# Optimization experiments

Measured on AMD Instinct MI355X. Metric: run time of the kernel, lower is better.

The kernel has to match this reference:

```python
import jax, jax.numpy as jnp
import numpy as np

B, L, DIM, HEADS = 4, 1024, 512, 8
HD = DIM // HEADS
HID = max(64, DIM // 2)
WIN = 32
SPARSITY = 0.3
TEMP = 1.0
PAT_TAU = 0.5


def setup_inputs() -> dict:
    key = jax.random.key(0)
    ks = jax.random.split(key, 8)
    gn = lambda k, shape, sc: jax.random.normal(k, shape, jnp.float32) * sc
    return {
        "x": jax.random.normal(ks[0], (B, L, DIM), jnp.float32),
        "mask": jnp.ones((B, L), jnp.int32),
        "Wqkv": gn(ks[1], (3 * DIM, DIM), 0.02),
        "Wproj": gn(ks[2], (DIM, DIM), 0.02),
        "bproj": jnp.zeros((DIM,), jnp.float32),
        "Wsel1": gn(ks[3], (HID, DIM), 0.05),
        "bsel1": jnp.zeros((HID,), jnp.float32),
        "Wsel2": gn(ks[4], (3, HID), 0.05),
        "bsel2": jnp.zeros((3,), jnp.float32),
        "log_pattern_tau": jnp.asarray(np.log(PAT_TAU), jnp.float32),
        "sparse_w": gn(ks[5], (HEADS,), 0.2),
        "sparse_b": jnp.zeros((HEADS,), jnp.float32),
    }


def reference(x, mask, Wqkv, Wproj, bproj, Wsel1, bsel1, Wsel2, bsel2,
              log_pattern_tau, sparse_w, sparse_b):
    Bq, Lq, D = x.shape
    scale = HD ** -0.5
    qkv = (x @ Wqkv.T).reshape(Bq, Lq, 3, HEADS, HD)
    q = jnp.transpose(qkv[:, :, 0], (0, 2, 1, 3))  # (B,H,L,hd)
    k = jnp.transpose(qkv[:, :, 1], (0, 2, 1, 3))
    v = jnp.transpose(qkv[:, :, 2], (0, 2, 1, 3))
    scores = jnp.einsum('bhid,bhjd->bhij', q, k) * scale  # (B,H,L,L)

    # pattern selector on mean-pooled features (eval: no gumbel, no dropout)
    pooled = x.mean(axis=1)
    logits = jax.nn.relu(pooled @ Wsel1.T + bsel1) @ Wsel2.T + bsel2  # (B,3)
    tau = jnp.clip(jnp.exp(log_pattern_tau), 1e-4, 10.0)
    pw = jax.nn.softmax(logits / tau, axis=-1)  # (B,3)

    half = WIN // 2
    ii = jnp.arange(Lq)[:, None]
    jj = jnp.arange(Lq)[None, :]
    local = ((jj >= ii - half) & (jj <= ii + half)).astype(jnp.float32)

    # learned sparse top-k mask per head via kth-value threshold
    kk = max(1, int(Lq * (1.0 - SPARSITY)))
    s = scores * sparse_w[None, :, None, None] + sparse_b[None, :, None, None]
    kth = jax.lax.top_k(s, kk)[0][..., -1:]
    smask = (s >= kth).astype(jnp.float32)  # (B,H,L,L)

    combined = (pw[:, 0, None, None, None] * local[None, None]
                + pw[:, 1, None, None, None]
                + pw[:, 2, None, None, None] * smask)
    neg = jnp.float32(-1e9)
    scores = jnp.where(combined > 0.05, scores, neg)
    scores = jnp.where(mask[:, None, None, :] == 0, neg, scores)

    # fallback: if a row is fully masked, unmask position 0
    all_masked = jnp.all(scores <= neg + 1e-6, axis=-1)  # (B,H,L)
    scores = scores.at[..., 0].set(jnp.where(all_masked, 0.0, scores[..., 0]))

    attn = jax.nn.softmax(scores / TEMP, axis=-1)
    out = jnp.einsum('bhij,bhjd->bhid', attn, v)
    out = jnp.transpose(out, (0, 2, 1, 3)).reshape(Bq, Lq, D)
    return out @ Wproj.T + bproj
```

## Files before the change

### kernel.cpp

```cpp
#include <hip/hip_runtime.h>
#include <math.h>

typedef __attribute__((ext_vector_type(8))) short short8;
typedef __attribute__((ext_vector_type(4))) float floatx4;

#define MFMA16(a, b, c) __builtin_amdgcn_mfma_f32_16x16x32_bf16(a, b, c, 0, 0, 0)

extern "C" __device__ float __ocml_native_exp2_f32(float);


#define FRAG512(row, k) (((size_t)((row) >> 4)) * 8192 + (((k) >> 5) * 512) + \
                         ((((k) >> 3) & 3) * 128) + (((row) & 15) * 8) + ((k) & 7))
#define FRAGQK(row, e)  (((size_t)((row) >> 4)) * 1024 + (((e) >> 5) * 512) + \
                         ((((e) >> 3) & 3) * 128) + (((row) & 15) * 8) + ((e) & 7))

#define OFF_XB    ((size_t)0)
#define OFF_WQKV  ((size_t)4194304)
#define OFF_WPROJ ((size_t)5767168)
#define OFF_Q     ((size_t)6291456)
#define OFF_K     ((size_t)10485760)
#define OFF_VT    ((size_t)14680064)
#define OFF_AT    ((size_t)18874368)
#define OFF_PW    ((size_t)23068672)
#define OFF_PAR   ((size_t)23069696)
#define OFF_W1T   ((size_t)23595008)

__device__ __forceinline__ unsigned short f2bf(float f) {
    unsigned u = __float_as_uint(f);
    return (unsigned short)((u + 0x7fffu + ((u >> 16) & 1u)) >> 16);
}
__device__ __forceinline__ float bf2f(unsigned short s) {
    return __uint_as_float((unsigned)s << 16);
}
__device__ __forceinline__ unsigned cvt_pk_bf16(float lo, float hi) {
    unsigned r;
    asm("v_cvt_pk_bf16_f32 %0, %1, %2" : "=v"(r) : "v"(lo), "v"(hi));
    return r;
}
__device__ __forceinline__ void gl16(const void* g, void* l) {
    __builtin_amdgcn_global_load_lds(
        (const __attribute__((address_space(1))) unsigned*)g,
        (__attribute__((address_space(3))) unsigned*)l, 16, 0, 0);
}

__device__ __forceinline__ void frag_cvt_tile(const float* __restrict__ src,
                                              unsigned short* __restrict__ dst,
                                              const int t, const float sc)
{
    const int ln = t & 15, quad = (t >> 4) & 3, kh = t >> 6;
    #pragma unroll
    for (int i = 0; i < 4; ++i) {
        const int kb = kh + i * 4;
        const float* s = src + (size_t)ln * 512 + kb * 32 + quad * 8;
        float4 f0 = *(const float4*)s;
        float4 f1 = *(const float4*)(s + 4);
        unsigned o01 = cvt_pk_bf16(f0.x * sc, f0.y * sc);
        unsigned o23 = cvt_pk_bf16(f0.z * sc, f0.w * sc);
        unsigned o45 = cvt_pk_bf16(f1.x * sc, f1.y * sc);
        unsigned o67 = cvt_pk_bf16(f1.z * sc, f1.w * sc);
        unsigned short* d = dst + kb * 512 + (size_t)(t & 63) * 8;
        *(uint2*)d       = make_uint2(o01, o23);
        *(uint2*)(d + 4) = make_uint2(o45, o67);
    }
}

__global__ __launch_bounds__(256)
void cvt_all(const float* __restrict__ x, const float* __restrict__ wqkv,
             const float* __restrict__ wproj, const float* __restrict__ W1,
             unsigned short* __restrict__ xb, unsigned short* __restrict__ oq,
             unsigned short* __restrict__ op, float* __restrict__ partial,
             float* __restrict__ w1t)
{
    const int bid = blockIdx.x, t = threadIdx.x;
    if (bid < 256) {
        const int rt = bid;
        const float* src = x + (size_t)rt * 16 * 512;
        frag_cvt_tile(src, xb + (size_t)rt * 8192, t, 1.f);
        float s0 = 0.f, s1 = 0.f;
        #pragma unroll 4
        for (int l = 0; l < 16; ++l) {
            s0 += src[(size_t)l * 512 + t];
            s1 += src[(size_t)l * 512 + t + 256];
        }
        partial[(size_t)rt * 512 + t] = s0;
        partial[(size_t)rt * 512 + t + 256] = s1;
    } else if (bid < 384) {
        const int tile = bid - 256;
        if (tile < 96)
            frag_cvt_tile(wqkv + (size_t)tile * 16 * 512, oq + (size_t)tile * 8192, t, 1.f);
        else
            frag_cvt_tile(wproj + (size_t)(tile - 96) * 16 * 512,
                          op + (size_t)(tile - 96) * 8192, t, 1.f);
    } else {
        __shared__ float tl[64][65];
        const int tile = bid - 384;
        const int tr = tile >> 3, tc = tile & 7;
        const int lr = t >> 6, lc = t & 63;
        #pragma unroll
        for (int p = 0; p < 16; ++p) {
            const int r = p * 4 + lr;
            tl[r][lc] = W1[(size_t)(tr * 64 + r) * 512 + tc * 64 + lc];
        }
        __syncthreads();
        #pragma unroll
        for (int p = 0; p < 16; ++p) {
            const int d = p * 4 + lr;
            w1t[(size_t)(tc * 64 + d) * 256 + tr * 64 + lc] = tl[lc][d];
        }
    }
}

__global__ __launch_bounds__(128)
void gemm_qkv_sel(const unsigned short* __restrict__ xb, const unsigned short* __restrict__ wb,
                  unsigned short* __restrict__ qo, unsigned short* __restrict__ ko,
                  unsigned short* __restrict__ vo,
                  const float* __restrict__ partial, const float* __restrict__ w1t,
                  const float* __restrict__ b1, const float* __restrict__ W2,
                  const float* __restrict__ b2, const float* __restrict__ ltau,
                  float* __restrict__ pwout)
{
    __shared__ __align__(16) unsigned short tile[2][64 * 72];
    const int bx = blockIdx.x, by = blockIdx.y;
    const int t = threadIdx.x;
    const int w = t >> 6, l64 = t & 63;

    if (by == 64) {
        if (bx >= 4) return;
        const int b = bx;
        float* pooled = (float*)&tile[0][0];
        float* hpart  = pooled + 512;
        float* h1s    = hpart + 512;
        float* lg     = h1s + 256;
        #pragma unroll
        for (int c = 0; c < 4; ++c) {
            const int col = t + c * 128;
            float s = 0.f;
            for (int p = 0; p < 64; ++p) s += partial[((size_t)b * 64 + p) * 512 + col];
            pooled[col] = s * (1.f / 1024.f);
        }
        __syncthreads();
        {
            float4 acc = make_float4(0.f, 0.f, 0.f, 0.f);
            const float* wt = w1t + (size_t)w * 256 * 256 + l64 * 4;
            for (int d = 0; d < 256; ++d) {
                const float pv = pooled[w * 256 + d];
                float4 wv = *(const float4*)(wt + (size_t)d * 256);
                acc.x += pv * wv.x; acc.y += pv * wv.y;
                acc.z += pv * wv.z; acc.w += pv * wv.w;
            }
            *(float4*)&hpart[w * 256 + l64 * 4] = acc;
        }
        __syncthreads();
        {
            #pragma unroll
            for (int c = 0; c < 2; ++c) {
                const int r = t + c * 128;
                h1s[r] = fmaxf(hpart[r] + hpart[256 + r] + b1[r], 0.f);
            }
        }
        __syncthreads();
        if (t < 3) {
            float s = b2[t];
            const float* w2 = W2 + t * 256;
            for (int i = 0; i < 256; ++i) s += w2[i] * h1s[i];
            float tauv = fminf(fmaxf(expf(ltau[0]), 1e-4f), 10.f);
            lg[t] = s / tauv;
        }
        __syncthreads();
        if (t == 0) {
            float m = fmaxf(lg[0], fmaxf(lg[1], lg[2]));
            float e0 = expf(lg[0] - m), e1 = expf(lg[1] - m), e2 = expf(lg[2] - m);
            float inv = 1.f / (e0 + e1 + e2);
            pwout[b * 3 + 0] = e0 * inv;
            pwout[b * 3 + 1] = e1 * inv;
            pwout[b * 3 + 2] = e2 * inv;
        }
        return;
    }

    const int ln = l64 & 15, quad = l64 >> 4;
    const int m0 = by << 6;
    const int nb0 = (bx << 7) + (w << 6);

    const unsigned short* Abase = xb + ((size_t)(m0 >> 4)) * 8192 + l64 * 8;
    const unsigned short* Bbase = wb + ((size_t)(nb0 >> 4)) * 8192 + l64 * 8;

    floatx4 acc[4][4];
    #pragma unroll
    for (int i = 0; i < 4; ++i)
        #pragma unroll
        for (int j = 0; j < 4; ++j) acc[i][j] = (floatx4){0.f, 0.f, 0.f, 0.f};

    short8 a0[4], b0[4], a1[4], b1v[4];
    #pragma unroll
    for (int i = 0; i < 4; ++i) {
        a0[i] = *(const short8*)(Abase + (size_t)i * 8192);
        b0[i] = *(const short8*)(Bbase + (size_t)i * 8192);
    }
    for (int s = 0; s < 16; s += 2) {
        #pragma unroll
        for (int i = 0; i < 4; ++i) {
            a1[i]  = *(const short8*)(Abase + (size_t)i * 8192 + (s + 1) * 512);
            b1v[i] = *(const short8*)(Bbase + (size_t)i * 8192 + (s + 1) * 512);
        }
        #pragma unroll
        for (int i = 0; i < 4; ++i)
            #pragma unroll
            for (int j = 0; j < 4; ++j)
                acc[i][j] = MFMA16(a0[i], b0[j], acc[i][j]);
        if (s + 2 < 16) {
            #pragma unroll
            for (int i = 0; i < 4; ++i) {
                a0[i] = *(const short8*)(Abase + (size_t)i * 8192 + (s + 2) * 512);
                b0[i] = *(const short8*)(Bbase + (size_t)i * 8192 + (s + 2) * 512);
            }
        }
        #pragma unroll
        for (int i = 0; i < 4; ++i)
            #pragma unroll
            for (int j = 0; j < 4; ++j)
                acc[i][j] = MFMA16(a1[i], b1v[j], acc[i][j]);
    }

    unsigned short* tw = &tile[w][0];
    const int which = bx >> 2;
    const int hh = (nb0 >> 6) & 7;
    const int g = (by >> 4) * 8 + hh;
    const int lrow0 = m0 & 1023;

    if (which == 2) {
        #pragma unroll
        for (int j = 0; j < 4; ++j)
            #pragma unroll
            for (int i = 0; i < 4; ++i) {
                unsigned u01 = cvt_pk_bf16(acc[i][j][0], acc[i][j][1]);
                unsigned u23 = cvt_pk_bf16(acc[i][j][2], acc[i][j][3]);
                *(uint2*)&tw[(j * 16 + ln) * 72 + i * 16 + quad * 4] = make_uint2(u01, u23);
            }
        const int chunk = lrow0 >> 7;
        const int ks0 = (lrow0 & 127) >> 5;
        unsigned short* dst = vo + (size_t)g * 65536 + (size_t)chunk * 8192;
        #pragma unroll
        for (int et = 0; et < 4; ++et)
            #pragma unroll
            for (int ksl = 0; ksl < 2; ++ksl) {
                const unsigned short* srcp = &tw[(et * 16 + ln) * 72 + ksl * 32 + quad * 8];
                *(short8*)(dst + (et * 4 + ks0 + ksl) * 512 + l64 * 8) = *(const short8*)srcp;
            }
    } else {
        const float sc = (which == 0) ? 0.180336880f : 1.f;
        #pragma unroll
        for (int j = 0; j < 4; ++j)
            #pragma unroll
            for (int i = 0; i < 4; ++i) {
                unsigned u01 = cvt_pk_bf16(acc[i][j][0] * sc, acc[i][j][1] * sc);
                unsigned u23 = cvt_pk_bf16(acc[i][j][2] * sc, acc[i][j][3] * sc);
                const int rb = (i * 16 + quad * 4) * 72 + j * 16 + ln;
                tw[rb]           = (unsigned short)u01;
                tw[rb + 72]      = (unsigned short)(u01 >> 16);
                tw[rb + 144]     = (unsigned short)u23;
                tw[rb + 216]     = (unsigned short)(u23 >> 16);
            }
        unsigned short* dst = (which == 0 ? qo : ko) + (size_t)g * 65536;
        #pragma unroll
        for (int rt = 0; rt < 4; ++rt)
            #pragma unroll
            for (int eh = 0; eh < 2; ++eh) {
                const unsigned short* srcp = &tw[(rt * 16 + ln) * 72 + eh * 32 + quad * 8];
                *(short8*)(dst + ((size_t)((lrow0 >> 4) + rt)) * 1024 + eh * 512 + l64 * 8) =
                    *(const short8*)srcp;
            }
    }
}

__global__ __launch_bounds__(64)
void gemm_proj(const unsigned short* __restrict__ ab, const unsigned short* __restrict__ wb,
               const float* __restrict__ bias, float* __restrict__ out)
{
    const int t = threadIdx.x;
    const int ln = t & 15, quad = t >> 4;
    const int n0 = blockIdx.x << 6, m0 = blockIdx.y << 5;

    const unsigned short* Abase = ab + ((size_t)(m0 >> 4)) * 8192 + t * 8;
    const unsigned short* Bbase = wb + ((size_t)(n0 >> 4)) * 8192 + t * 8;

    floatx4 acc[2][4];
    #pragma unroll
    for (int i = 0; i < 2; ++i)
        #pragma unroll
        for (int j = 0; j < 4; ++j) acc[i][j] = (floatx4){0.f, 0.f, 0.f, 0.f};

    short8 a0[2], b0[4], a1[2], b1v[4];
    #pragma unroll
    for (int i = 0; i < 2; ++i) a0[i] = *(const short8*)(Abase + (size_t)i * 8192);
    #pragma unroll
    for (int j = 0; j < 4; ++j) b0[j] = *(const short8*)(Bbase + (size_t)j * 8192);
    for (int s = 0; s < 16; s += 2) {
        #pragma unroll
        for (int i = 0; i < 2; ++i) a1[i]  = *(const short8*)(Abase + (size_t)i * 8192 + (s + 1) * 512);
        #pragma unroll
        for (int j = 0; j < 4; ++j) b1v[j] = *(const short8*)(Bbase + (size_t)j * 8192 + (s + 1) * 512);
        #pragma unroll
        for (int i = 0; i < 2; ++i)
            #pragma unroll
            for (int j = 0; j < 4; ++j)
                acc[i][j] = MFMA16(a0[i], b0[j], acc[i][j]);
        if (s + 2 < 16) {
            #pragma unroll
            for (int i = 0; i < 2; ++i) a0[i] = *(const short8*)(Abase + (size_t)i * 8192 + (s + 2) * 512);
            #pragma unroll
            for (int j = 0; j < 4; ++j) b0[j] = *(const short8*)(Bbase + (size_t)j * 8192 + (s + 2) * 512);
        }
        #pragma unroll
        for (int i = 0; i < 2; ++i)
            #pragma unroll
            for (int j = 0; j < 4; ++j)
                acc[i][j] = MFMA16(a1[i], b1v[j], acc[i][j]);
    }
    #pragma unroll
    for (int j = 0; j < 4; ++j) {
        const float bv = bias[n0 + j * 16 + ln];
        #pragma unroll
        for (int i = 0; i < 2; ++i)
            #pragma unroll
            for (int reg = 0; reg < 4; ++reg)
                out[(size_t)(m0 + i * 16 + quad * 4 + reg) * 512 + n0 + j * 16 + ln] =
                    acc[i][j][reg] + bv;
    }
}

__global__ __launch_bounds__(256)
void attn_flash(const unsigned short* __restrict__ qm, const unsigned short* __restrict__ km,
                const unsigned short* __restrict__ vm, const int* __restrict__ mask,
                const float* __restrict__ pw, const float* __restrict__ sw,
                const float* __restrict__ sb, unsigned short* __restrict__ aout)
{
    __shared__ int mk[1024];
    __shared__ __align__(16) unsigned short Ks[2][8192];
    __shared__ __align__(16) unsigned short Vs[8192];
    __shared__ __align__(16) unsigned short Pws[4][2176];
    __shared__ unsigned kths[4][16];

    const int t = threadIdx.x;
    const int w = t >> 6, l64 = t & 63;
    const int ln = l64 & 15, quad = l64 >> 4;
    const int g = blockIdx.x & 31;
    const int rg = blockIdx.x >> 5;
    const int b = g >> 3, h = g & 7;
    const int i0 = rg * 64 + w * 16;

    const unsigned short* qg = qm + (size_t)g * 65536;
    const unsigned short* kg = km + (size_t)g * 65536;
    const unsigned short* vg = vm + (size_t)g * 65536;

    *(int4*)&mk[t * 4] = *(const int4*)(mask + b * 1024 + t * 4);

    const float pw0 = pw[b * 3 + 0], pw1 = pw[b * 3 + 1], pw2 = pw[b * 3 + 2];
    const bool a00 = pw1 > 0.05f;
    const bool a10 = (pw0 * 1.0f + pw1) > 0.05f;
    const bool a01 = (pw1 + pw2) > 0.05f;
    const bool a11 = ((pw0 * 1.0f + pw1) + pw2) > 0.05f;
    const bool need_sparse = (!a00 && a01) || (!a10 && a11);
    const bool flat_ok = (!need_sparse) && a00 && a10;
    const float w_h = sw[h], b_h = sb[h];

    #pragma unroll
    for (int c = 0; c < 4; ++c) {
        const int bi = w * 4 + c;
        gl16(kg + bi * 512 + l64 * 8, (char*)Ks[0] + bi * 1024);
    }

    unsigned kth_r[4] = {0u, 0u, 0u, 0u};
    if (need_sparse) {
        unsigned* ub = (unsigned*)((char*)Ks + 16384 + w * 4096);
        for (int r = 0; r < 16; ++r) {
            for (int c = 0; c < 16; ++c) {
                const int col = c * 64 + l64;
                float s = 0.f;
                for (int e = 0; e < 64; ++e)
                    s += bf2f(qg[FRAGQK(i0 + r, e)]) * bf2f(kg[FRAGQK(col, e)]);
                unsigned uu = __float_as_uint(s * w_h + b_h);
                ub[col] = (uu & 0x80000000u) ? ~uu : (uu | 0x80000000u);
            }
            unsigned u[16];
            #pragma unroll
            for (int c = 0; c < 16; ++c) u[c] = ub[l64 + c * 64];
            unsigned act = 0xFFFFu, p = 0u;
            int kk = 716;
            for (int bit = 31; bit >= 0; --bit) {
                unsigned ones = 0u;
                #pragma unroll
                for (int c = 0; c < 16; ++c)
                    if (((act >> c) & 1u) && ((u[c] >> bit) & 1u)) ones |= (1u << c);
                int c1 = __popc(ones);
                for (int off = 32; off; off >>= 1) c1 += __shfl_xor(c1, off);
                if (kk <= c1) { p |= (1u << bit); act &= ones; }
                else          { kk -= c1; act &= ~ones; }
            }
            if (l64 == 0) kths[w][r] = p;
        }
        #pragma unroll
        for (int reg = 0; reg < 4; ++reg) kth_r[reg] = kths[w][quad * 4 + reg];
    }

    const short8 aq0 = *(const short8*)(qg + ((size_t)(i0 >> 4)) * 1024 + l64 * 8);
    const short8 aq1 = *(const short8*)(qg + ((size_t)(i0 >> 4)) * 1024 + 512 + l64 * 8);

    __syncthreads();

    float l_acc[4] = {0.f, 0.f, 0.f, 0.f};
    floatx4 accv[4];
    #pragma unroll
    for (int et = 0; et < 4; ++et) accv[et] = (floatx4){0.f, 0.f, 0.f, 0.f};
    unsigned short* Pw = &Pws[w][0];

    for (int jc = 0; jc < 8; ++jc) {
        const int j0 = jc << 7;
        const int cur = jc & 1;
        const unsigned short* Kc = &Ks[cur][0];
        {
            const unsigned short* vc = vg + (size_t)jc * 8192;
            #pragma unroll
            for (int c = 0; c < 4; ++c) {
                const int bi = w * 4 + c;
                gl16(vc + bi * 512 + l64 * 8, (char*)Vs + bi * 1024);
            }
            if (jc < 7) {
                const unsigned short* kc = kg + (size_t)(jc + 1) * 8192;
                #pragma unroll
                for (int c = 0; c < 4; ++c) {
                    const int bi = w * 4 + c;
                    gl16(kc + bi * 512 + l64 * 8, (char*)Ks[cur ^ 1] + bi * 1024);
                }
            }
        }
        const bool mall = __all((mk[j0 + l64] != 0) && (mk[j0 + 64 + l64] != 0));
        const bool fast = flat_ok && mall;

        floatx4 sfr[8];
        #pragma unroll
        for (int nt = 0; nt < 8; ++nt) {
            const short8 kb0 = *(const short8*)(Kc + nt * 1024 + l64 * 8);
            const short8 kb1 = *(const short8*)(Kc + nt * 1024 + 512 + l64 * 8);
            floatx4 z = (floatx4){0.f, 0.f, 0.f, 0.f};
            z = MFMA16(aq0, kb0, z);
            z = MFMA16(aq1, kb1, z);
            sfr[nt] = z;
        }

        if (!fast) {
            #pragma unroll
            for (int nt = 0; nt < 8; ++nt) {
                const int j = j0 + nt * 16 + ln;
                const bool mk0 = (mk[j] == 0);
                #pragma unroll
                for (int reg = 0; reg < 4; ++reg) {
                    const int i = i0 + quad * 4 + reg;
                    const float s = sfr[nt][reg];
                    const bool loc = (j >= i - 16) && (j <= i + 16);
                    bool sm = false;
                    if (need_sparse) {
                        unsigned uu = __float_as_uint(s * w_h + b_h);
                        unsigned key = (uu & 0x80000000u) ? ~uu : (uu | 0x80000000u);
                        sm = key >= kth_r[reg];
                    }
                    bool allowed = loc ? (sm ? a11 : a10) : (sm ? a01 : a00);
                    if (mk0) allowed = false;
                    sfr[nt][reg] = allowed ? s : -1e9f;
                }
            }
        }
        #pragma unroll
        for (int nt = 0; nt < 8; ++nt) {
            const float p0 = __ocml_native_exp2_f32(sfr[nt][0]);
            const float p1 = __ocml_native_exp2_f32(sfr[nt][1]);
            const float p2 = __ocml_native_exp2_f32(sfr[nt][2]);
            const float p3 = __ocml_native_exp2_f32(sfr[nt][3]);
            l_acc[0] += p0; l_acc[1] += p1; l_acc[2] += p2; l_acc[3] += p3;
            const unsigned u01 = cvt_pk_bf16(p0, p1);
            const unsigned u23 = cvt_pk_bf16(p2, p3);
            const int col = nt * 16 + ln;
            Pw[(quad * 4 + 0) * 136 + col] = (unsigned short)u01;
            Pw[(quad * 4 + 1) * 136 + col] = (unsigned short)(u01 >> 16);
            Pw[(quad * 4 + 2) * 136 + col] = (unsigned short)u23;
            Pw[(quad * 4 + 3) * 136 + col] = (unsigned short)(u23 >> 16);
        }
        short8 pa[4];
        #pragma unroll
        for (int ks = 0; ks < 4; ++ks)
            pa[ks] = *(const short8*)&Pw[ln * 136 + ks * 32 + quad * 8];
        __syncthreads();
        #pragma unroll
        for (int et = 0; et < 4; ++et) {
            floatx4 a = accv[et];
            #pragma unroll
            for (int ks = 0; ks < 4; ++ks) {
                const short8 bv = *(const short8*)(Vs + (et * 4 + ks) * 512 + l64 * 8);
                a = MFMA16(pa[ks], bv, a);
            }
            accv[et] = a;
        }
        __syncthreads();
    }

    #pragma unroll
    for (int reg = 0; reg < 4; ++reg) {
        float v = l_acc[reg];
        v += __shfl_xor(v, 1);
        v += __shfl_xor(v, 2);
        v += __shfl_xor(v, 4);
        v += __shfl_xor(v, 8);
        l_acc[reg] = v;
    }

    float* PO_w = (float*)((char*)Ks + w * 4352);
    #pragma unroll
    for (int et = 0; et < 4; ++et)
        #pragma unroll
        for (int reg = 0; reg < 4; ++reg) {
            float val;
            if (l_acc[reg] == 0.f)
                val = bf2f(vg[et * 2048 + ln * 8]);
            else
                val = accv[et][reg] / l_acc[reg];
            PO_w[(quad * 4 + reg) * 68 + et * 16 + ln] = val;
        }
    #pragma unroll
    for (int rr = 0; rr < 4; ++rr) {
        const int r = (l64 >> 4) * 4 + rr;
        const int cb = (l64 & 15) * 4;
        float4 ov = *(const float4*)&PO_w[r * 68 + cb];
        const unsigned uxy = cvt_pk_bf16(ov.x, ov.y);
        const unsigned uzw = cvt_pk_bf16(ov.z, ov.w);
        const int row_g = b * 1024 + i0 + r;
        const int col = h * 64 + cb;
        *(uint2*)&aout[FRAG512(row_g, col)] = make_uint2(uxy, uzw);
    }
}

extern "C" void kernel_launch(void* const* d_in, const int* in_sizes, int n_in,
                              void* d_out, int out_size, void* d_ws, size_t ws_size,
                              hipStream_t stream) {
    const float* x     = (const float*)d_in[0];
    const int*   mask  = (const int*)d_in[1];
    const float* Wqkv  = (const float*)d_in[2];
    const float* Wproj = (const float*)d_in[3];
    const float* bproj = (const float*)d_in[4];
    const float* Wsel1 = (const float*)d_in[5];
    const float* bsel1 = (const float*)d_in[6];
    const float* Wsel2 = (const float*)d_in[7];
    const float* bsel2 = (const float*)d_in[8];
    const float* ltau  = (const float*)d_in[9];
    const float* sw    = (const float*)d_in[10];
    const float* sb    = (const float*)d_in[11];
    char* ws = (char*)d_ws;
    unsigned short* xb     = (unsigned short*)(ws + OFF_XB);
    unsigned short* wqkvb  = (unsigned short*)(ws + OFF_WQKV);
    unsigned short* wprojb = (unsigned short*)(ws + OFF_WPROJ);
    unsigned short* q      = (unsigned short*)(ws + OFF_Q);
    unsigned short* k      = (unsigned short*)(ws + OFF_K);
    unsigned short* v      = (unsigned short*)(ws + OFF_VT);
    unsigned short* attnb  = (unsigned short*)(ws + OFF_AT);
    float* pw  = (float*)(ws + OFF_PW);
    float* par = (float*)(ws + OFF_PAR);
    float* w1t = (float*)(ws + OFF_W1T);
    float* out = (float*)d_out;
    (void)in_sizes; (void)n_in; (void)out_size; (void)ws_size;

    cvt_all<<<416, 256, 0, stream>>>(x, Wqkv, Wproj, Wsel1, xb, wqkvb, wprojb, par, w1t);
    gemm_qkv_sel<<<dim3(12, 65), 128, 0, stream>>>(xb, wqkvb, q, k, v,
                                                   par, w1t, bsel1, Wsel2, bsel2, ltau, pw);
    attn_flash<<<512, 256, 0, stream>>>(q, k, v, mask, pw, sw, sb, attnb);
    gemm_proj<<<dim3(8, 128), 64, 0, stream>>>(attnb, wprojb, bproj, out);
}
```

Before: 143.7 us.

## Enlarge QKV GEMM blocks to 128x128 and swizzle workgroup order for XCD locality

The QKV GEMM now runs 256-thread blocks, each covering a 128x128 output tile with four waves in a 2x2 layout, which halves the grid. The selector MLP branch is adapted to the wider block. Both the QKV and projection GEMMs remap the linear workgroup id so that consecutive ids spread across the 8 XCDs and neighbouring tiles share an L2, aiming at better cache reuse of A and B. Since waves read fragments straight from global memory, the larger block mainly changes scheduling and cache locality, not register-level reuse.

```diff
diff --git a/kernel.cpp b/kernel.cpp
--- a/kernel.cpp
+++ b/kernel.cpp
@@ -110,7 +110,7 @@
     }
 }
 
-__global__ __launch_bounds__(128)
+__global__ __launch_bounds__(256)
 void gemm_qkv_sel(const unsigned short* __restrict__ xb, const unsigned short* __restrict__ wb,
                   unsigned short* __restrict__ qo, unsigned short* __restrict__ ko,
                   unsigned short* __restrict__ vo,
@@ -119,21 +119,20 @@
                   const float* __restrict__ b2, const float* __restrict__ ltau,
                   float* __restrict__ pwout)
 {
-    __shared__ __align__(16) unsigned short tile[2][64 * 72];
-    const int bx = blockIdx.x, by = blockIdx.y;
+    __shared__ __align__(16) unsigned short tile[4][64 * 72];
     const int t = threadIdx.x;
     const int w = t >> 6, l64 = t & 63;
 
-    if (by == 64) {
-        if (bx >= 4) return;
-        const int b = bx;
+    if (blockIdx.y == 32) {
+        if (blockIdx.x >= 4) return;
+        const int b = blockIdx.x;
         float* pooled = (float*)&tile[0][0];
         float* hpart  = pooled + 512;
-        float* h1s    = hpart + 512;
+        float* h1s    = hpart + 1024;
         float* lg     = h1s + 256;
         #pragma unroll
-        for (int c = 0; c < 4; ++c) {
-            const int col = t + c * 128;
+        for (int c = 0; c < 2; ++c) {
+            const int col = t + c * 256;
             float s = 0.f;
             for (int p = 0; p < 64; ++p) s += partial[((size_t)b * 64 + p) * 512 + col];
             pooled[col] = s * (1.f / 1024.f);
@@ -141,9 +140,9 @@
         __syncthreads();
         {
             float4 acc = make_float4(0.f, 0.f, 0.f, 0.f);
-            const float* wt = w1t + (size_t)w * 256 * 256 + l64 * 4;
-            for (int d = 0; d < 256; ++d) {
-                const float pv = pooled[w * 256 + d];
+            const float* wt = w1t + (size_t)w * 128 * 256 + l64 * 4;
+            for (int d = 0; d < 128; ++d) {
+                const float pv = pooled[w * 128 + d];
                 float4 wv = *(const float4*)(wt + (size_t)d * 256);
                 acc.x += pv * wv.x; acc.y += pv * wv.y;
                 acc.z += pv * wv.z; acc.w += pv * wv.w;
@@ -151,13 +150,7 @@
             *(float4*)&hpart[w * 256 + l64 * 4] = acc;
         }
         __syncthreads();
-        {
-            #pragma unroll
-            for (int c = 0; c < 2; ++c) {
-                const int r = t + c * 128;
-                h1s[r] = fmaxf(hpart[r] + hpart[256 + r] + b1[r], 0.f);
-            }
-        }
+        h1s[t] = fmaxf(hpart[t] + hpart[256 + t] + hpart[512 + t] + hpart[768 + t] + b1[t], 0.f);
         __syncthreads();
         if (t < 3) {
             float s = b2[t];
@@ -178,9 +171,13 @@
         return;
     }
 
+    const int wg = blockIdx.y * 12 + blockIdx.x;
+    const int sw_id = (wg & 7) * 48 + (wg >> 3);
+    const int bx = sw_id % 12, by = sw_id / 12;
+
     const int ln = l64 & 15, quad = l64 >> 4;
-    const int m0 = by << 6;
-    const int nb0 = (bx << 7) + (w << 6);
+    const int m0  = (by << 7) + ((w >> 1) << 6);
+    const int nb0 = (bx << 7) + ((w & 1) << 6);
 
     const unsigned short* Abase = xb + ((size_t)(m0 >> 4)) * 8192 + l64 * 8;
     const unsigned short* Bbase = wb + ((size_t)(nb0 >> 4)) * 8192 + l64 * 8;
@@ -223,9 +220,9 @@
     }
 
     unsigned short* tw = &tile[w][0];
-    const int which = bx >> 2;
+    const int which = nb0 >> 9;
     const int hh = (nb0 >> 6) & 7;
-    const int g = (by >> 4) * 8 + hh;
+    const int g = (m0 >> 10) * 8 + hh;
     const int lrow0 = m0 & 1023;
 
     if (which == 2) {
@@ -279,7 +276,9 @@
 {
     const int t = threadIdx.x;
     const int ln = t & 15, quad = t >> 4;
-    const int n0 = blockIdx.x << 6, m0 = blockIdx.y << 5;
+    const int wg = blockIdx.y * 8 + blockIdx.x;
+    const int sw_id = (wg & 7) * 128 + (wg >> 3);
+    const int n0 = (sw_id & 7) << 6, m0 = (sw_id >> 3) << 5;
 
     const unsigned short* Abase = ab + ((size_t)(m0 >> 4)) * 8192 + t * 8;
     const unsigned short* Bbase = wb + ((size_t)(n0 >> 4)) * 8192 + t * 8;
@@ -568,7 +567,7 @@
     (void)in_sizes; (void)n_in; (void)out_size; (void)ws_size;
 
     cvt_all<<<416, 256, 0, stream>>>(x, Wqkv, Wproj, Wsel1, xb, wqkvb, wprojb, par, w1t);
-    gemm_qkv_sel<<<dim3(12, 65), 128, 0, stream>>>(xb, wqkvb, q, k, v,
+    gemm_qkv_sel<<<dim3(12, 33), 256, 0, stream>>>(xb, wqkvb, q, k, v,
                                                    par, w1t, bsel1, Wsel2, bsel2, ltau, pw);
     attn_flash<<<512, 256, 0, stream>>>(q, k, v, mask, pw, sw, sb, attnb);
     gemm_proj<<<dim3(8, 128), 64, 0, stream>>>(attnb, wprojb, bproj, out);
```

Result: faster. 135.1 us (-6.0%).
